# Optimization experiments

Measured on AMD Instinct MI355X. Metric: run time of the kernel, lower is better.

The kernel has to match this reference:

```python
import jax, jax.numpy as jnp
import numpy as np

B, S, D = 8, 1024, 1024
H = 16
DH = D // H
DFF = 4096
L = 2
EPS = 1e-6


def setup_inputs() -> dict:
    key = jax.random.key(0)
    ks = jax.random.split(key, 12)
    sc = 0.02
    x = jax.random.normal(ks[0], (B, S, D), dtype=jnp.float32)
    # causal mask: 1 where position j > i (masked), broadcast over batch/head
    mask = jnp.triu(jnp.ones((S, S), dtype=jnp.float32), k=1)[None, None]
    Wq = jax.random.normal(ks[1], (L, D, D), dtype=jnp.float32) * sc
    Wk = jax.random.normal(ks[2], (L, D, D), dtype=jnp.float32) * sc
    Wv = jax.random.normal(ks[3], (L, D, D), dtype=jnp.float32) * sc
    Wo = jax.random.normal(ks[4], (L, D, D), dtype=jnp.float32) * sc
    bq = jnp.zeros((L, D), jnp.float32)
    bk = jnp.zeros((L, D), jnp.float32)
    bv = jnp.zeros((L, D), jnp.float32)
    bo = jnp.zeros((L, D), jnp.float32)
    W1 = jax.random.normal(ks[5], (L, D, DFF), dtype=jnp.float32) * sc
    b1 = jnp.zeros((L, DFF), jnp.float32)
    W2 = jax.random.normal(ks[6], (L, DFF, D), dtype=jnp.float32) * sc
    b2 = jnp.zeros((L, D), jnp.float32)
    ln1_g = jnp.ones((L, D), jnp.float32)
    ln1_b = jnp.zeros((L, D), jnp.float32)
    ln2_g = jnp.ones((L, D), jnp.float32)
    ln2_b = jnp.zeros((L, D), jnp.float32)
    return dict(x=x, mask=mask, Wq=Wq, bq=bq, Wk=Wk, bk=bk, Wv=Wv, bv=bv,
                Wo=Wo, bo=bo, W1=W1, b1=b1, W2=W2, b2=b2,
                ln1_g=ln1_g, ln1_b=ln1_b, ln2_g=ln2_g, ln2_b=ln2_b)


def layer_norm(x, g, b):
    mu = jnp.mean(x, axis=-1, keepdims=True)
    var = jnp.mean(jnp.square(x - mu), axis=-1, keepdims=True)
    return (x - mu) * jax.lax.rsqrt(var + EPS) * g + b


def reference(x, mask, Wq, bq, Wk, bk, Wv, bv, Wo, bo, W1, b1, W2, b2,
              ln1_g, ln1_b, ln2_g, ln2_b):
    scale = 1.0 / jnp.sqrt(jnp.float32(DH))
    for l in range(L):
        # --- multi-head attention (inference mode: no dropout) ---
        q = (x @ Wq[l] + bq[l]).reshape(B, S, H, DH).transpose(0, 2, 1, 3)
        k = (x @ Wk[l] + bk[l]).reshape(B, S, H, DH).transpose(0, 2, 1, 3)
        v = (x @ Wv[l] + bv[l]).reshape(B, S, H, DH).transpose(0, 2, 1, 3)
        sim = jnp.einsum('bhqd,bhkd->bhqk', q, k) * scale + mask * (-1e9)
        attn = jax.nn.softmax(sim, axis=-1)
        o = jnp.einsum('bhqk,bhkd->bhqd', attn, v)
        o = o.transpose(0, 2, 1, 3).reshape(B, S, D)
        o = o @ Wo[l] + bo[l]
        x = layer_norm(o + x, ln1_g[l], ln1_b[l])
        # --- feed-forward network ---
        h = jax.nn.relu(x @ W1[l] + b1[l])
        f = h @ W2[l] + b2[l]
        x = layer_norm(x + f, ln2_g[l], ln2_b[l])
    return x
```

## Files before the change

### kernel.cpp

```cpp
#include <hip/hip_runtime.h>

typedef __attribute__((ext_vector_type(8))) short bf16x8;
typedef __attribute__((ext_vector_type(4))) float f32x4;
typedef unsigned short ushort_t;
typedef unsigned int uint32;

#define DEV __device__ __forceinline__

DEV ushort_t f2bf(float f) {
    uint32 u = __float_as_uint(f);
    uint32 r = (u + 0x7FFFu + ((u >> 16) & 1u)) >> 16;
    return (ushort_t)r;
}
DEV float bf2f(ushort_t h) { return __uint_as_float(((uint32)h) << 16); }

#define MFMA16(a, b, c) __builtin_amdgcn_mfma_f32_16x16x32_bf16((a), (b), (c), 0, 0, 0)

DEV void gload_lds16(const void* g, void* l) {
    __builtin_amdgcn_global_load_lds((const __attribute__((address_space(1))) void*)g,
                                     (__attribute__((address_space(3))) void*)l,
                                     16, 0, 0);
}

__global__ __launch_bounds__(256) void init_x(const float* __restrict__ xin,
                                              ushort_t* __restrict__ xr, int n4) {
    int i = blockIdx.x * 256 + threadIdx.x;
    if (i >= n4) return;
    float4 v = ((const float4*)xin)[i];
    ushort4 h;
    h.x = f2bf(v.x); h.y = f2bf(v.y); h.z = f2bf(v.z); h.w = f2bf(v.w);
    ((ushort4*)xr)[i] = h;
}

__global__ __launch_bounds__(256) void transpose_all(const float* __restrict__ Wq,
                                                     const float* __restrict__ Wk,
                                                     const float* __restrict__ Wv,
                                                     const float* __restrict__ Wo,
                                                     const float* __restrict__ W1,
                                                     const float* __restrict__ W2,
                                                     ushort_t* __restrict__ wqkvT,
                                                     ushort_t* __restrict__ woT,
                                                     ushort_t* __restrict__ w1T,
                                                     ushort_t* __restrict__ w2T) {
    const int l = blockIdx.y;
    const int t = blockIdx.x;
    const float* src;
    ushort_t* dst;
    int K, N, ktile, ntile;
    if (t < 4096) {
        const int which = t >> 10, tile = t & 1023;
        K = 1024; N = 1024; ktile = tile >> 5; ntile = tile & 31;
        const size_t o1 = (size_t)l * 1048576;
        if (which == 0)      { src = Wq + o1; dst = wqkvT + (size_t)l * 3145728; }
        else if (which == 1) { src = Wk + o1; dst = wqkvT + (size_t)l * 3145728 + 1048576; }
        else if (which == 2) { src = Wv + o1; dst = wqkvT + (size_t)l * 3145728 + 2097152; }
        else                 { src = Wo + o1; dst = woT + o1; }
    } else if (t < 8192) {
        const int tile = t - 4096;
        K = 1024; N = 4096; ktile = tile >> 7; ntile = tile & 127;
        src = W1 + (size_t)l * 4194304; dst = w1T + (size_t)l * 4194304;
    } else {
        const int tile = t - 8192;
        K = 4096; N = 1024; ktile = tile >> 5; ntile = tile & 31;
        src = W2 + (size_t)l * 4194304; dst = w2T + (size_t)l * 4194304;
    }
    __shared__ float tilebuf[32][33];
    const int tx = threadIdx.x, ty = threadIdx.y;
    const int nt = ntile * 32, kt = ktile * 32;
#pragma unroll
    for (int j = 0; j < 4; ++j)
        tilebuf[ty + j * 8][tx] = src[(size_t)(kt + ty + j * 8) * N + nt + tx];
    __syncthreads();
#pragma unroll
    for (int j = 0; j < 4; ++j)
        dst[(size_t)(nt + ty + j * 8) * K + kt + tx] = f2bf(tilebuf[tx][ty + j * 8]);
}

template <int BM, int MODE, int RELU>
__global__ __launch_bounds__(512, 2) void gemm8p(const ushort_t* __restrict__ A,
                                                 const ushort_t* __restrict__ BT,
                                                 const float* __restrict__ bias,
                                                 void* __restrict__ Cout,
                                                 int M, int N, int K, int gx,
                                                 ushort_t* __restrict__ qout,
                                                 ushort_t* __restrict__ kout,
                                                 ushort_t* __restrict__ vtout,
                                                 const float* __restrict__ bq,
                                                 const float* __restrict__ bk,
                                                 const float* __restrict__ bv) {
    constexpr int AH = BM / 128;
    constexpr int MREP = BM / 32;
    constexpr int PHASES = (BM == 128) ? 2 : 4;
    constexpr int MPP = MREP / PHASES;
    __shared__ ushort_t lds[2][(BM + 256) * 64];

    const int nwg = gridDim.x;
    const int q8 = nwg >> 3, r8 = nwg & 7;
    const int xcd = blockIdx.x & 7, idx = blockIdx.x >> 3;
    const int swz = (xcd < r8 ? xcd * (q8 + 1) : r8 * (q8 + 1) + (xcd - r8) * q8) + idx;
    const int bxi = swz % gx, byi = swz / gx;

    const int tid = threadIdx.x;
    const int w = tid >> 6, lane = tid & 63;
    const int wr = w >> 2, wc = w & 3;
    const int lr = lane & 15, lh = lane >> 4;
    const int row0 = byi * BM, col0 = bxi * 256;

    f32x4 acc[MREP][4] = {};

    const ushort_t* __restrict__ Ab = A + (size_t)row0 * K;
    const ushort_t* __restrict__ Bb = BT + (size_t)col0 * K;
    const int nt = K >> 6;

    const int r8l = lane >> 3;
    const int cu = (lane & 7) ^ r8l;
    const int so = w * 1024 + lane * 8;

    const ushort_t* aS[AH][2];
    const ushort_t* bS[2][2];
#pragma unroll
    for (int h2 = 0; h2 < AH; ++h2)
#pragma unroll
        for (int i = 0; i < 2; ++i)
            aS[h2][i] = Ab + (size_t)(h2 * 128 + (w * 2 + i) * 8 + r8l) * K + cu * 8;
#pragma unroll
    for (int h2 = 0; h2 < 2; ++h2)
#pragma unroll
        for (int i = 0; i < 2; ++i)
            bS[h2][i] = Bb + (size_t)(h2 * 128 + (w * 2 + i) * 8 + r8l) * K + cu * 8;

    auto stageA = [&](int buf, int h2) {
#pragma unroll
        for (int i = 0; i < 2; ++i) {
            gload_lds16(aS[h2][i], &lds[buf][h2 * 8192 + so + i * 512]);
            aS[h2][i] += 64;
        }
    };
    auto stageB = [&](int buf, int h2) {
#pragma unroll
        for (int i = 0; i < 2; ++i) {
            gload_lds16(bS[h2][i], &lds[buf][BM * 64 + h2 * 8192 + so + i * 512]);
            bS[h2][i] += 64;
        }
    };

    int boff[4][2];
#pragma unroll
    for (int ni = 0; ni < 4; ++ni) {
        const int br = wc * 64 + ni * 16 + lr;
        const int rr = br & 127, bh2 = br >> 7;
#pragma unroll
        for (int ks = 0; ks < 2; ++ks)
            boff[ni][ks] = BM * 64 + bh2 * 8192 + rr * 64 + (((ks * 4 + lh) ^ (rr & 7)) * 8);
    }
    int aoff[MREP][2];
#pragma unroll
    for (int mi = 0; mi < MREP; ++mi) {
        const int fr = wr * (BM / 2) + mi * 16 + lr;
        const int rr = fr & 127, fh = fr >> 7;
#pragma unroll
        for (int ks = 0; ks < 2; ++ks)
            aoff[mi][ks] = fh * 8192 + rr * 64 + (((ks * 4 + lh) ^ (rr & 7)) * 8);
    }

    stageB(0, 0); stageB(0, 1);
    stageA(0, 0); if (AH == 2) stageA(0, 1);
    stageB(1, 0); stageB(1, 1);
    asm volatile("s_waitcnt vmcnt(4)" ::: "memory");
    __builtin_amdgcn_sched_barrier(0);
    __builtin_amdgcn_s_barrier();

    for (int t2 = 0; t2 < nt; t2 += 2) {
#pragma unroll
        for (int ti = 0; ti < 2; ++ti) {
            const int t = t2 + ti;
            bf16x8 bfrag[4][2];
#pragma unroll
            for (int p = 0; p < PHASES; ++p) {
                if (p == 0) {
#pragma unroll
                    for (int ni = 0; ni < 4; ++ni)
#pragma unroll
                        for (int ks = 0; ks < 2; ++ks)
                            bfrag[ni][ks] = *(const bf16x8*)&lds[ti][boff[ni][ks]];
                }
                bf16x8 af[MPP][2];
#pragma unroll
                for (int mm = 0; mm < MPP; ++mm)
#pragma unroll
                    for (int ks = 0; ks < 2; ++ks)
                        af[mm][ks] = *(const bf16x8*)&lds[ti][aoff[p * MPP + mm][ks]];
                if (PHASES == 4) {
                    if (p == 0) { if (t + 1 < nt) stageA(1 - ti, 0); }
                    else if (p == 1) { if (AH == 2 && t + 1 < nt) stageA(1 - ti, 1); }
                    else if (p == 2) { if (t + 2 < nt) stageB(ti, 0); }
                    else {
                        if (t + 2 < nt) {
                            stageB(ti, 1);
                            asm volatile("s_waitcnt vmcnt(4)" ::: "memory");
                        } else if (t + 1 < nt) {
                            asm volatile("s_waitcnt vmcnt(0)" ::: "memory");
                        }
                    }
                } else {
                    if (p == 0) { if (t + 1 < nt) stageA(1 - ti, 0); }
                    else {
                        if (t + 2 < nt) {
                            stageB(ti, 0);
                            stageB(ti, 1);
                            asm volatile("s_waitcnt vmcnt(4)" ::: "memory");
                        } else if (t + 1 < nt) {
                            asm volatile("s_waitcnt vmcnt(0)" ::: "memory");
                        }
                    }
                }
                __builtin_amdgcn_sched_barrier(0);
                __builtin_amdgcn_s_barrier();
                asm volatile("s_waitcnt lgkmcnt(0)" ::: "memory");
                __builtin_amdgcn_sched_barrier(0);
                __builtin_amdgcn_s_setprio(1);
#pragma unroll
                for (int mm = 0; mm < MPP; ++mm)
#pragma unroll
                    for (int ni = 0; ni < 4; ++ni)
#pragma unroll
                        for (int ks = 0; ks < 2; ++ks)
                            acc[p * MPP + mm][ni] = MFMA16(af[mm][ks], bfrag[ni][ks], acc[p * MPP + mm][ni]);
                __builtin_amdgcn_s_setprio(0);
                __builtin_amdgcn_sched_barrier(0);
                __builtin_amdgcn_s_barrier();
            }
        }
    }
    (void)M;

    if (MODE == 2 && col0 >= 2048) {
        ushort_t* vb = &lds[0][0] + w * 4096;
        const int hglob = (col0 - 2048 + wc * 64) >> 6;
        const int bidx = row0 >> 10;
        const int srow0 = (row0 & 1023) + wr * 64;
#pragma unroll
        for (int mi = 0; mi < MREP; ++mi) {
#pragma unroll
            for (int ni = 0; ni < 4; ++ni) {
                const int dd = ni * 16 + lr;
                const float bvv = bv[(hglob << 6) + dd];
                ushort4 h4;
                h4.x = f2bf(acc[mi][ni][0] + bvv);
                h4.y = f2bf(acc[mi][ni][1] + bvv);
                h4.z = f2bf(acc[mi][ni][2] + bvv);
                h4.w = f2bf(acc[mi][ni][3] + bvv);
                const int sb = mi * 32 + lh * 8;
                *(ushort4*)((char*)vb + dd * 128 + (sb ^ ((dd & 3) << 4))) = h4;
            }
        }
        const int ddl = lane >> 3, s8 = lane & 7;
#pragma unroll
        for (int j = 0; j < 8; ++j) {
            const int dd = j * 8 + ddl;
            bf16x8 rowv = *(const bf16x8*)((char*)vb + dd * 128 + ((s8 * 16) ^ ((dd & 3) << 4)));
            *(bf16x8*)&vtout[(((size_t)(bidx * 16 + hglob) * 64 + dd) << 10) + srow0 + s8 * 8] = rowv;
        }
    } else {
#pragma unroll
        for (int mi = 0; mi < MREP; ++mi) {
#pragma unroll
            for (int ni = 0; ni < 4; ++ni) {
                const int col = col0 + wc * 64 + ni * 16 + lr;
                const int rowb = row0 + wr * (BM / 2) + mi * 16 + lh * 4;
                if (MODE == 2) {
                    if (col < 1024) {
                        const float bvv = bq[col];
#pragma unroll
                        for (int r = 0; r < 4; ++r)
                            qout[(size_t)(rowb + r) * 1024 + col] = f2bf((acc[mi][ni][r] + bvv) * 0.125f);
                    } else {
                        const int c = col - 1024;
                        const float bvv = bk[c];
#pragma unroll
                        for (int r = 0; r < 4; ++r)
                            kout[(size_t)(rowb + r) * 1024 + c] = f2bf(acc[mi][ni][r] + bvv);
                    }
                } else {
                    const float bvv = bias[col];
#pragma unroll
                    for (int r = 0; r < 4; ++r) {
                        float val = acc[mi][ni][r] + bvv;
                        if (RELU) val = fmaxf(val, 0.f);
                        ((ushort_t*)Cout)[(size_t)(rowb + r) * N + col] = f2bf(val);
                    }
                }
            }
        }
    }
}

__global__ __launch_bounds__(256) void attn_kernel(const ushort_t* __restrict__ q,
                                                   const ushort_t* __restrict__ k,
                                                   const ushort_t* __restrict__ vt,
                                                   ushort_t* __restrict__ o) {
    __shared__ ushort_t ktile[64 * 64];
    __shared__ ushort_t vtile[64 * 64];
    __shared__ ushort_t p_lds[4][16 * 64];

    const int bh = blockIdx.x;
    const int b = bh >> 4, h = bh & 15;
    const int qt = blockIdx.y;
    const int tid = threadIdx.x, w = tid >> 6, lane = tid & 63;
    const int lr = lane & 15, lh = lane >> 4;
    const int qbase = qt * 64 + w * 16;
    const size_t headoff = (size_t)b * 1024 * 1024 + h * 64;
    const size_t vhead = (size_t)(b * 16 + h) << 16;

    bf16x8 qf[2];
#pragma unroll
    for (int ks = 0; ks < 2; ++ks)
        qf[ks] = *(const bf16x8*)&q[headoff + (size_t)(qbase + lr) * 1024 + ks * 32 + lh * 8];

    f32x4 oacc[4] = {};
    float m[4] = {-INFINITY, -INFINITY, -INFINITY, -INFINITY};
    float ls[4] = {0.f, 0.f, 0.f, 0.f};

    const int srow = tid >> 3;
    const int scolb = (tid & 7) * 16;
    const int swz0 = ((srow & 7) << 4);
    char* const kbase = (char*)ktile;
    char* const vbase = (char*)vtile;
    char* const kw0 = kbase + srow * 128 + (scolb ^ swz0);
    char* const kw1 = kbase + (srow + 32) * 128 + (scolb ^ swz0);
    char* const vw0 = vbase + srow * 128 + (scolb ^ swz0);
    char* const vw1 = vbase + (srow + 32) * 128 + (scolb ^ swz0);
    const ushort_t* kg = k + headoff + (size_t)srow * 1024 + (tid & 7) * 8;
    const ushort_t* vg = vt + vhead + (size_t)srow * 1024 + (tid & 7) * 8;

    const int jmaxw = qbase + 15;
    const int jend = qt * 64 + 63;

    bf16x8 sk0 = *(const bf16x8*)&kg[0];
    bf16x8 sk1 = *(const bf16x8*)&kg[32 * 1024];
    bf16x8 sv0 = *(const bf16x8*)&vg[0];
    bf16x8 sv1 = *(const bf16x8*)&vg[32 * 1024];

    for (int j0 = 0; j0 <= jend; j0 += 64) {
        __syncthreads();
        *(bf16x8*)kw0 = sk0;
        *(bf16x8*)kw1 = sk1;
        *(bf16x8*)vw0 = sv0;
        *(bf16x8*)vw1 = sv1;
        __syncthreads();
        if (j0 + 64 <= jend) {
            sk0 = *(const bf16x8*)&kg[(size_t)(j0 + 64) * 1024];
            sk1 = *(const bf16x8*)&kg[(size_t)(j0 + 64) * 1024 + 32 * 1024];
            sv0 = *(const bf16x8*)&vg[j0 + 64];
            sv1 = *(const bf16x8*)&vg[32 * 1024 + j0 + 64];
        }

        if (j0 <= jmaxw) {
            f32x4 s[4] = {{0,0,0,0},{0,0,0,0},{0,0,0,0},{0,0,0,0}};
#pragma unroll
            for (int kt = 0; kt < 4; ++kt) {
                const int row = kt * 16 + lr;
                const int rswz = ((row & 7) << 4);
#pragma unroll
                for (int ks = 0; ks < 2; ++ks) {
                    bf16x8 kf = *(const bf16x8*)(kbase + row * 128 + ((ks * 64 + lh * 16) ^ rswz));
                    s[kt] = MFMA16(qf[ks], kf, s[kt]);
                }
            }
            if (j0 + 63 > qbase) {
#pragma unroll
                for (int kt = 0; kt < 4; ++kt)
#pragma unroll
                    for (int r = 0; r < 4; ++r)
                        s[kt][r] = ((j0 + kt * 16 + lr) <= (qbase + lh * 4 + r)) ? s[kt][r] : -1e9f;
            }
#pragma unroll
            for (int r = 0; r < 4; ++r) {
                float pm = fmaxf(fmaxf(s[0][r], s[1][r]), fmaxf(s[2][r], s[3][r]));
                pm = fmaxf(pm, __shfl_xor(pm, 1, 16));
                pm = fmaxf(pm, __shfl_xor(pm, 2, 16));
                pm = fmaxf(pm, __shfl_xor(pm, 4, 16));
                pm = fmaxf(pm, __shfl_xor(pm, 8, 16));
                const float mn = fmaxf(m[r], pm);
                const float corr = __expf(m[r] - mn);
                m[r] = mn;
                float p0 = __expf(s[0][r] - mn);
                float p1 = __expf(s[1][r] - mn);
                float p2 = __expf(s[2][r] - mn);
                float p3 = __expf(s[3][r] - mn);
                s[0][r] = p0; s[1][r] = p1; s[2][r] = p2; s[3][r] = p3;
                float ps = (p0 + p1) + (p2 + p3);
                ps += __shfl_xor(ps, 1, 16);
                ps += __shfl_xor(ps, 2, 16);
                ps += __shfl_xor(ps, 4, 16);
                ps += __shfl_xor(ps, 8, 16);
                ls[r] = ls[r] * corr + ps;
                oacc[0][r] *= corr; oacc[1][r] *= corr;
                oacc[2][r] *= corr; oacc[3][r] *= corr;
            }
            char* const pb = (char*)p_lds[w];
#pragma unroll
            for (int r = 0; r < 4; ++r) {
                const int qrow = lh * 4 + r;
                const int qswz = ((qrow & 7) << 4);
#pragma unroll
                for (int kt = 0; kt < 4; ++kt)
                    *(ushort_t*)(pb + qrow * 128 + ((kt * 32 + lr * 2) ^ qswz)) = f2bf(s[kt][r]);
            }
            const int pswz = ((lr & 7) << 4);
            bf16x8 pa0 = *(const bf16x8*)(pb + lr * 128 + ((lh * 16) ^ pswz));
            bf16x8 pa1 = *(const bf16x8*)(pb + lr * 128 + ((64 + lh * 16) ^ pswz));
#pragma unroll
            for (int dt = 0; dt < 4; ++dt) {
                const int vrow = dt * 16 + lr;
                const int vswz = ((vrow & 7) << 4);
                bf16x8 vf0 = *(const bf16x8*)(vbase + vrow * 128 + ((lh * 16) ^ vswz));
                oacc[dt] = MFMA16(pa0, vf0, oacc[dt]);
                bf16x8 vf1 = *(const bf16x8*)(vbase + vrow * 128 + ((64 + lh * 16) ^ vswz));
                oacc[dt] = MFMA16(pa1, vf1, oacc[dt]);
            }
        }
    }

    float inv[4];
#pragma unroll
    for (int r = 0; r < 4; ++r) inv[r] = 1.f / ls[r];
#pragma unroll
    for (int dt = 0; dt < 4; ++dt)
#pragma unroll
        for (int r = 0; r < 4; ++r) {
            const int row = qbase + lh * 4 + r;
            o[headoff + (size_t)row * 1024 + dt * 16 + lr] = f2bf(oacc[dt][r] * inv[r]);
        }
}

template <int LAST>
__global__ __launch_bounds__(256) void add_ln(const ushort_t* __restrict__ t,
                                              ushort_t* __restrict__ xr,
                                              const float* __restrict__ g,
                                              const float* __restrict__ bb,
                                              float* __restrict__ out) {
    const int row = blockIdx.x, tid = threadIdx.x;
    const int lane = tid & 63, w = tid >> 6;
    const size_t base = (size_t)row * 1024;
    ushort4 tv = ((const ushort4*)(t + base))[tid];
    ushort4 xv = ((const ushort4*)(xr + base))[tid];
    float v0 = bf2f(tv.x) + bf2f(xv.x), v1 = bf2f(tv.y) + bf2f(xv.y);
    float v2 = bf2f(tv.z) + bf2f(xv.z), v3 = bf2f(tv.w) + bf2f(xv.w);
    float s = v0 + v1 + v2 + v3;
    float sq = v0 * v0 + v1 * v1 + v2 * v2 + v3 * v3;
#pragma unroll
    for (int off = 32; off >= 1; off >>= 1) {
        s += __shfl_xor(s, off);
        sq += __shfl_xor(sq, off);
    }
    __shared__ float red[8];
    if (lane == 0) { red[w] = s; red[4 + w] = sq; }
    __syncthreads();
    s = red[0] + red[1] + red[2] + red[3];
    sq = red[4] + red[5] + red[6] + red[7];
    const float mu = s * (1.f / 1024.f);
    const float var = sq * (1.f / 1024.f) - mu * mu;
    const float rs = rsqrtf(var + 1e-6f);
    float4 gv = ((const float4*)g)[tid];
    float4 bv = ((const float4*)bb)[tid];
    float y0 = (v0 - mu) * rs * gv.x + bv.x;
    float y1 = (v1 - mu) * rs * gv.y + bv.y;
    float y2 = (v2 - mu) * rs * gv.z + bv.z;
    float y3 = (v3 - mu) * rs * gv.w + bv.w;
    if (LAST) {
        float4 yo; yo.x = y0; yo.y = y1; yo.z = y2; yo.w = y3;
        ((float4*)(out + base))[tid] = yo;
    } else {
        ushort4 hh;
        hh.x = f2bf(y0); hh.y = f2bf(y1); hh.z = f2bf(y2); hh.w = f2bf(y3);
        ((ushort4*)(xr + base))[tid] = hh;
    }
}

extern "C" void kernel_launch(void* const* d_in, const int* in_sizes, int n_in,
                              void* d_out, int out_size, void* d_ws, size_t ws_size,
                              hipStream_t stream) {
    (void)in_sizes; (void)n_in; (void)out_size; (void)ws_size;
    const int B = 8, S = 1024, D = 1024, DFF = 4096, L = 2;
    const int M = B * S;

    const float* x_in = (const float*)d_in[0];
    const float* Wq = (const float*)d_in[2];
    const float* bq = (const float*)d_in[3];
    const float* Wk = (const float*)d_in[4];
    const float* bk = (const float*)d_in[5];
    const float* Wv = (const float*)d_in[6];
    const float* bv = (const float*)d_in[7];
    const float* Wo = (const float*)d_in[8];
    const float* bo = (const float*)d_in[9];
    const float* W1 = (const float*)d_in[10];
    const float* b1 = (const float*)d_in[11];
    const float* W2 = (const float*)d_in[12];
    const float* b2 = (const float*)d_in[13];
    const float* ln1g = (const float*)d_in[14];
    const float* ln1b = (const float*)d_in[15];
    const float* ln2g = (const float*)d_in[16];
    const float* ln2b = (const float*)d_in[17];

    float* out = (float*)d_out;
    char* ws = (char*)d_ws;
    const size_t MB = 1024 * 1024;
    ushort_t* wqkvT = (ushort_t*)(ws + 0 * MB);
    ushort_t* woT = (ushort_t*)(ws + 12 * MB);
    ushort_t* w1T = (ushort_t*)(ws + 16 * MB);
    ushort_t* w2T = (ushort_t*)(ws + 32 * MB);
    ushort_t* xr  = (ushort_t*)(ws + 48 * MB);
    ushort_t* qb  = (ushort_t*)(ws + 64 * MB);
    ushort_t* kb  = (ushort_t*)(ws + 80 * MB);
    ushort_t* vtb = (ushort_t*)(ws + 96 * MB);
    ushort_t* ob  = (ushort_t*)(ws + 112 * MB);
    ushort_t* hb  = (ushort_t*)(ws + 64 * MB);
    ushort_t* tb  = (ushort_t*)(ws + 128 * MB);

    init_x<<<M * D / 4 / 256, 256, 0, stream>>>(x_in, xr, M * D / 4);
    transpose_all<<<dim3(12288, L), dim3(32, 8), 0, stream>>>(
        Wq, Wk, Wv, Wo, W1, W2, wqkvT, woT, w1T, w2T);

    for (int l = 0; l < L; ++l) {
        const size_t wOff = (size_t)l * D * D;
        const size_t bOff = (size_t)l * D;
        gemm8p<128, 2, 0><<<dim3(768), 512, 0, stream>>>(
            xr, wqkvT + (size_t)l * 3 * D * D, nullptr, nullptr, M, 3 * D, D, 12,
            qb, kb, vtb, bq + bOff, bk + bOff, bv + bOff);
        attn_kernel<<<dim3(B * 16, S / 64), 256, 0, stream>>>(qb, kb, vtb, ob);
        gemm8p<128, 1, 0><<<dim3(256), 512, 0, stream>>>(
            ob, woT + wOff, bo + bOff, tb, M, D, D, 4,
            nullptr, nullptr, nullptr, nullptr, nullptr, nullptr);
        add_ln<0><<<M, 256, 0, stream>>>(tb, xr, ln1g + bOff, ln1b + bOff, nullptr);
        gemm8p<256, 1, 1><<<dim3(512), 512, 0, stream>>>(
            xr, w1T + (size_t)l * D * DFF, b1 + (size_t)l * DFF, hb, M, DFF, D, 16,
            nullptr, nullptr, nullptr, nullptr, nullptr, nullptr);
        gemm8p<128, 1, 0><<<dim3(256), 512, 0, stream>>>(
            hb, w2T + (size_t)l * DFF * D, b2 + bOff, tb, M, D, DFF, 4,
            nullptr, nullptr, nullptr, nullptr, nullptr, nullptr);
        if (l == L - 1)
            add_ln<1><<<M, 256, 0, stream>>>(tb, xr, ln2g + bOff, ln2b + bOff, out);
        else
            add_ln<0><<<M, 256, 0, stream>>>(tb, xr, ln2g + bOff, ln2b + bOff, nullptr);
    }
}
```

Baseline: 679.9 us.

## Widen attention KV tile to 128 keys and shrink FFN1 GEMM tile

The attention kernel now processes 128 keys per iteration instead of 64. That halves the number of loop iterations, barriers and online-softmax rescale steps, and widens the K/V/P shared-memory tiles with an adjusted XOR swizzle. Separately, the first FFN GEMM switches from a 256 to a 128 tile template with twice as many blocks. The trade-offs are more registers and LDS per attention block, more wasted causal-masked work on diagonal tiles, and possibly less reuse in the FFN GEMM.

```diff
diff --git a/kernel.cpp b/kernel.cpp
--- a/kernel.cpp
+++ b/kernel.cpp
@@ -299,9 +299,9 @@
                                                    const ushort_t* __restrict__ k,
                                                    const ushort_t* __restrict__ vt,
                                                    ushort_t* __restrict__ o) {
-    __shared__ ushort_t ktile[64 * 64];
-    __shared__ ushort_t vtile[64 * 64];
-    __shared__ ushort_t p_lds[4][16 * 64];
+    __shared__ ushort_t ktile[128 * 64];
+    __shared__ ushort_t vtile[64 * 128];
+    __shared__ ushort_t p_lds[4][16 * 128];
 
     const int bh = blockIdx.x;
     const int b = bh >> 4, h = bh & 15;
@@ -322,61 +322,71 @@
     float ls[4] = {0.f, 0.f, 0.f, 0.f};
 
     const int srow = tid >> 3;
-    const int scolb = (tid & 7) * 16;
-    const int swz0 = ((srow & 7) << 4);
+    const int scol8 = (tid & 7) * 8;
     char* const kbase = (char*)ktile;
     char* const vbase = (char*)vtile;
-    char* const kw0 = kbase + srow * 128 + (scolb ^ swz0);
-    char* const kw1 = kbase + (srow + 32) * 128 + (scolb ^ swz0);
-    char* const vw0 = vbase + srow * 128 + (scolb ^ swz0);
-    char* const vw1 = vbase + (srow + 32) * 128 + (scolb ^ swz0);
-    const ushort_t* kg = k + headoff + (size_t)srow * 1024 + (tid & 7) * 8;
-    const ushort_t* vg = vt + vhead + (size_t)srow * 1024 + (tid & 7) * 8;
+    const int kswzb = (scol8 * 2) ^ ((srow & 7) << 4);
+    const int vswzr = ((srow & 15) << 4);
+    const ushort_t* kg = k + headoff + (size_t)srow * 1024 + scol8;
+    const ushort_t* vg = vt + vhead + (size_t)srow * 1024 + scol8;
 
     const int jmaxw = qbase + 15;
     const int jend = qt * 64 + 63;
 
-    bf16x8 sk0 = *(const bf16x8*)&kg[0];
-    bf16x8 sk1 = *(const bf16x8*)&kg[32 * 1024];
-    bf16x8 sv0 = *(const bf16x8*)&vg[0];
-    bf16x8 sv1 = *(const bf16x8*)&vg[32 * 1024];
-
-    for (int j0 = 0; j0 <= jend; j0 += 64) {
+    bf16x8 sk[4], sv[4];
+#pragma unroll
+    for (int p = 0; p < 4; ++p) sk[p] = *(const bf16x8*)&kg[(size_t)(p * 32) * 1024];
+#pragma unroll
+    for (int p = 0; p < 2; ++p)
+#pragma unroll
+        for (int kh = 0; kh < 2; ++kh)
+            sv[p * 2 + kh] = *(const bf16x8*)&vg[(size_t)(p * 32) * 1024 + kh * 64];
+
+    for (int j0 = 0; j0 <= jend; j0 += 128) {
         __syncthreads();
-        *(bf16x8*)kw0 = sk0;
-        *(bf16x8*)kw1 = sk1;
-        *(bf16x8*)vw0 = sv0;
-        *(bf16x8*)vw1 = sv1;
+#pragma unroll
+        for (int p = 0; p < 4; ++p)
+            *(bf16x8*)(kbase + (srow + 32 * p) * 128 + kswzb) = sk[p];
+#pragma unroll
+        for (int p = 0; p < 2; ++p)
+#pragma unroll
+            for (int kh = 0; kh < 2; ++kh)
+                *(bf16x8*)(vbase + (srow + 32 * p) * 256 + ((kh * 128 + scol8 * 2) ^ vswzr)) = sv[p * 2 + kh];
         __syncthreads();
-        if (j0 + 64 <= jend) {
-            sk0 = *(const bf16x8*)&kg[(size_t)(j0 + 64) * 1024];
-            sk1 = *(const bf16x8*)&kg[(size_t)(j0 + 64) * 1024 + 32 * 1024];
-            sv0 = *(const bf16x8*)&vg[j0 + 64];
-            sv1 = *(const bf16x8*)&vg[32 * 1024 + j0 + 64];
+        if (j0 + 128 <= jend) {
+#pragma unroll
+            for (int p = 0; p < 4; ++p)
+                sk[p] = *(const bf16x8*)&kg[(size_t)(j0 + 128 + p * 32) * 1024];
+#pragma unroll
+            for (int p = 0; p < 2; ++p)
+#pragma unroll
+                for (int kh = 0; kh < 2; ++kh)
+                    sv[p * 2 + kh] = *(const bf16x8*)&vg[(size_t)(p * 32) * 1024 + j0 + 128 + kh * 64];
         }
 
         if (j0 <= jmaxw) {
-            f32x4 s[4] = {{0,0,0,0},{0,0,0,0},{0,0,0,0},{0,0,0,0}};
-#pragma unroll
-            for (int kt = 0; kt < 4; ++kt) {
-                const int row = kt * 16 + lr;
-                const int rswz = ((row & 7) << 4);
+            f32x4 s[8] = {};
+#pragma unroll
+            for (int kt = 0; kt < 8; ++kt) {
+                const int krow = kt * 16 + lr;
+                const int rswz = ((krow & 7) << 4);
 #pragma unroll
                 for (int ks = 0; ks < 2; ++ks) {
-                    bf16x8 kf = *(const bf16x8*)(kbase + row * 128 + ((ks * 64 + lh * 16) ^ rswz));
+                    bf16x8 kf = *(const bf16x8*)(kbase + krow * 128 + ((ks * 64 + lh * 16) ^ rswz));
                     s[kt] = MFMA16(qf[ks], kf, s[kt]);
                 }
             }
-            if (j0 + 63 > qbase) {
-#pragma unroll
-                for (int kt = 0; kt < 4; ++kt)
+            if (j0 + 127 > qbase) {
+#pragma unroll
+                for (int kt = 0; kt < 8; ++kt)
 #pragma unroll
                     for (int r = 0; r < 4; ++r)
                         s[kt][r] = ((j0 + kt * 16 + lr) <= (qbase + lh * 4 + r)) ? s[kt][r] : -1e9f;
             }
 #pragma unroll
             for (int r = 0; r < 4; ++r) {
-                float pm = fmaxf(fmaxf(s[0][r], s[1][r]), fmaxf(s[2][r], s[3][r]));
+                float pm = fmaxf(fmaxf(fmaxf(s[0][r], s[1][r]), fmaxf(s[2][r], s[3][r])),
+                                 fmaxf(fmaxf(s[4][r], s[5][r]), fmaxf(s[6][r], s[7][r])));
                 pm = fmaxf(pm, __shfl_xor(pm, 1, 16));
                 pm = fmaxf(pm, __shfl_xor(pm, 2, 16));
                 pm = fmaxf(pm, __shfl_xor(pm, 4, 16));
@@ -384,12 +394,13 @@
                 const float mn = fmaxf(m[r], pm);
                 const float corr = __expf(m[r] - mn);
                 m[r] = mn;
-                float p0 = __expf(s[0][r] - mn);
-                float p1 = __expf(s[1][r] - mn);
-                float p2 = __expf(s[2][r] - mn);
-                float p3 = __expf(s[3][r] - mn);
-                s[0][r] = p0; s[1][r] = p1; s[2][r] = p2; s[3][r] = p3;
-                float ps = (p0 + p1) + (p2 + p3);
+                float ps = 0.f;
+#pragma unroll
+                for (int kt = 0; kt < 8; ++kt) {
+                    const float pv = __expf(s[kt][r] - mn);
+                    s[kt][r] = pv;
+                    ps += pv;
+                }
                 ps += __shfl_xor(ps, 1, 16);
                 ps += __shfl_xor(ps, 2, 16);
                 ps += __shfl_xor(ps, 4, 16);
@@ -402,22 +413,25 @@
 #pragma unroll
             for (int r = 0; r < 4; ++r) {
                 const int qrow = lh * 4 + r;
-                const int qswz = ((qrow & 7) << 4);
-#pragma unroll
-                for (int kt = 0; kt < 4; ++kt)
-                    *(ushort_t*)(pb + qrow * 128 + ((kt * 32 + lr * 2) ^ qswz)) = f2bf(s[kt][r]);
-            }
-            const int pswz = ((lr & 7) << 4);
-            bf16x8 pa0 = *(const bf16x8*)(pb + lr * 128 + ((lh * 16) ^ pswz));
-            bf16x8 pa1 = *(const bf16x8*)(pb + lr * 128 + ((64 + lh * 16) ^ pswz));
+                const int qswz = ((qrow & 15) << 4);
+#pragma unroll
+                for (int kt = 0; kt < 8; ++kt)
+                    *(ushort_t*)(pb + qrow * 256 + ((kt * 32 + lr * 2) ^ qswz)) = f2bf(s[kt][r]);
+            }
+            const int pswz = ((lr & 15) << 4);
+            bf16x8 pa[4];
+#pragma unroll
+            for (int ks = 0; ks < 4; ++ks)
+                pa[ks] = *(const bf16x8*)(pb + lr * 256 + ((ks * 64 + lh * 16) ^ pswz));
 #pragma unroll
             for (int dt = 0; dt < 4; ++dt) {
                 const int vrow = dt * 16 + lr;
-                const int vswz = ((vrow & 7) << 4);
-                bf16x8 vf0 = *(const bf16x8*)(vbase + vrow * 128 + ((lh * 16) ^ vswz));
-                oacc[dt] = MFMA16(pa0, vf0, oacc[dt]);
-                bf16x8 vf1 = *(const bf16x8*)(vbase + vrow * 128 + ((64 + lh * 16) ^ vswz));
-                oacc[dt] = MFMA16(pa1, vf1, oacc[dt]);
+                const int vswz = ((vrow & 15) << 4);
+#pragma unroll
+                for (int ks = 0; ks < 4; ++ks) {
+                    bf16x8 vf = *(const bf16x8*)(vbase + vrow * 256 + ((ks * 64 + lh * 16) ^ vswz));
+                    oacc[dt] = MFMA16(pa[ks], vf, oacc[dt]);
+                }
             }
         }
     }
@@ -533,7 +547,7 @@
             ob, woT + wOff, bo + bOff, tb, M, D, D, 4,
             nullptr, nullptr, nullptr, nullptr, nullptr, nullptr);
         add_ln<0><<<M, 256, 0, stream>>>(tb, xr, ln1g + bOff, ln1b + bOff, nullptr);
-        gemm8p<256, 1, 1><<<dim3(512), 512, 0, stream>>>(
+        gemm8p<128, 1, 1><<<dim3(1024), 512, 0, stream>>>(
             xr, w1T + (size_t)l * D * DFF, b1 + (size_t)l * DFF, hb, M, DFF, D, 16,
             nullptr, nullptr, nullptr, nullptr, nullptr, nullptr);
         gemm8p<128, 1, 0><<<dim3(256), 512, 0, stream>>>(
```

New measurement: 702.1 us. 1.03x slower.
